# Performance work log

Hardware: AMD Instinct MI355X
Metric: run time of the kernel (lower is better)

Reference implementation:

```python
import math
import jax, jax.numpy as jnp
import numpy as np

V, D, H, L, F, T, B = 32000, 1024, 16, 4, 4096, 1024, 2
HD = D // H
EPS = 1e-5


def make_pe(max_len, d):
    pos = np.arange(max_len)[:, None].astype(np.float32)
    div = np.exp(np.arange(0, d, 2).astype(np.float32) * (-math.log(10000.0) / d))
    pe = np.zeros((max_len, d), dtype=np.float32)
    pe[:, 0::2] = np.sin(pos * div)
    pe[:, 1::2] = np.cos(pos * div)
    return jnp.asarray(pe)


def setup_inputs() -> dict:
    key = jax.random.key(0)
    ks = jax.random.split(key, 12)
    s = 0.02
    inp = {
        'tokens': jax.random.randint(ks[0], (B, T), 0, V, dtype=jnp.int32),
        'mask': jnp.tril(jnp.ones((T, T), dtype=jnp.int32)),
        'emb': jax.random.normal(ks[1], (V, D), jnp.float32) * s,
        'pe': make_pe(T, D),
        'ln1_g': jnp.ones((L, D)), 'ln1_b': jnp.zeros((L, D)),
        'Wqkv': jax.random.normal(ks[2], (L, D, 3 * D), jnp.float32) * s,
        'bqkv': jnp.zeros((L, 3 * D)),
        'Wproj': jax.random.normal(ks[3], (L, D, D), jnp.float32) * s,
        'bproj': jnp.zeros((L, D)),
        'ln2_g': jnp.ones((L, D)), 'ln2_b': jnp.zeros((L, D)),
        'W1': jax.random.normal(ks[4], (L, D, F), jnp.float32) * s,
        'b1': jnp.zeros((L, F)),
        'W2': jax.random.normal(ks[5], (L, F, D), jnp.float32) * s,
        'b2': jnp.zeros((L, D)),
        'lnf_g': jnp.ones((D,)), 'lnf_b': jnp.zeros((D,)),
        'out_b': jnp.zeros((V,)),
    }
    return inp


def layer_norm(x, g, b):
    m = jnp.mean(x, axis=-1, keepdims=True)
    v = jnp.mean((x - m) ** 2, axis=-1, keepdims=True)
    return (x - m) / jnp.sqrt(v + EPS) * g + b


def attention(x, mask, Wqkv, bqkv, Wproj, bproj):
    b, t, c = x.shape
    qkv = (x @ Wqkv + bqkv).reshape(b, t, 3, H, HD)
    q, k, v = jnp.moveaxis(qkv, 2, 0)  # each [B,T,H,HD]
    q = q.transpose(0, 2, 1, 3)  # [B,H,T,HD]
    k = k.transpose(0, 2, 1, 3)
    v = v.transpose(0, 2, 1, 3)
    scores = jnp.einsum('bhqd,bhkd->bhqk', q, k) / math.sqrt(HD)
    scores = jnp.where(mask[None, None] == 0, -1e9, scores)
    attn = jax.nn.softmax(scores, axis=-1)
    out = jnp.einsum('bhqk,bhkd->bhqd', attn, v)
    out = out.transpose(0, 2, 1, 3).reshape(b, t, c)
    return out @ Wproj + bproj, attn


def reference(tokens, mask, emb, pe, ln1_g, ln1_b, Wqkv, bqkv, Wproj, bproj,
              ln2_g, ln2_b, W1, b1, W2, b2, lnf_g, lnf_b, out_b):
    x = emb[tokens] + pe[:tokens.shape[1]]
    attn = None
    for i in range(L):
        a, attn = attention(layer_norm(x, ln1_g[i], ln1_b[i]), mask,
                            Wqkv[i], bqkv[i], Wproj[i], bproj[i])
        x = x + a
        h = layer_norm(x, ln2_g[i], ln2_b[i])
        h = jax.nn.gelu(h @ W1[i] + b1[i], approximate=False) @ W2[i] + b2[i]
        x = x + h
    x = layer_norm(x, lnf_g, lnf_b)
    logits = x @ emb.T + out_b  # weight tying
    return logits, attn
```

## Files before the change

### kernel.cpp

```cpp
#include <hip/hip_runtime.h>
#include <cstdint>

#define DEV static __device__ __forceinline__

typedef unsigned short u16;
typedef __bf16 bf16x8 __attribute__((ext_vector_type(8)));
typedef float f32x4 __attribute__((ext_vector_type(4)));
typedef unsigned short u16x4 __attribute__((ext_vector_type(4)));

constexpr int V = 32000, D = 1024, H = 16, L = 4, F = 4096, T = 1024, B = 2;
constexpr int HD = 64;

DEV u16 f2bf(float f) {
    union { float f; uint32_t i; } c; c.f = f;
    uint32_t x = c.i;
    return (u16)((x + 0x7fffu + ((x >> 16) & 1u)) >> 16);
}
DEV float bf2f(u16 u) {
    union { uint32_t i; float f; } c; c.i = ((uint32_t)u) << 16; return c.f;
}
DEV bf16x8 ld8(const u16* p) { return *reinterpret_cast<const bf16x8*>(p); }

DEV void gl16(const void* g, void* l) {
    __builtin_amdgcn_global_load_lds((const __attribute__((address_space(1))) void*)g,
                                     (__attribute__((address_space(3))) void*)l, 16, 0, 0);
}

DEV void castT4_dev(int t, int x, int y, u16 (*tl)[33],
        const float* __restrict__ Wqkv, const float* __restrict__ Wproj,
        const float* __restrict__ W1, const float* __restrict__ W2,
        u16* __restrict__ wt) {
    const float* src; u16* dst; int Rr, Cc;
    if (t < 768)       { src = Wqkv;  dst = wt;                       Rr = D; Cc = 3 * D; }
    else if (t < 1024) { src = Wproj; dst = wt + 3 * D * D;           Rr = D; Cc = D; t -= 768; }
    else if (t < 2048) { src = W1;    dst = wt + 4 * D * D;           Rr = D; Cc = F; t -= 1024; }
    else               { src = W2;    dst = wt + 4 * D * D + D * F;   Rr = F; Cc = D; t -= 2048; }
    int colStrips = Cc >> 7;
    int r0 = (t / colStrips) * 32;
    int c0 = (t % colStrips) * 128;
    for (int i = 0; i < 4; i++) {
        int cc = c0 + i * 32;
        __syncthreads();
#pragma unroll
        for (int j = 0; j < 4; j++)
            tl[y + j * 8][x] = f2bf(src[(size_t)(r0 + y + j * 8) * Cc + cc + x]);
        __syncthreads();
#pragma unroll
        for (int j = 0; j < 4; j++)
            dst[(size_t)(cc + y + j * 8) * Rr + r0 + x] = tl[x][y + j * 8];
    }
}

__global__ __launch_bounds__(256) void k_emblnT(const int* __restrict__ tok,
        const float* __restrict__ emb, const float* __restrict__ pe,
        const float* __restrict__ g, const float* __restrict__ b,
        float* __restrict__ x, u16* __restrict__ out,
        const float* __restrict__ Wqkv, const float* __restrict__ Wproj,
        const float* __restrict__ W1, const float* __restrict__ W2,
        u16* __restrict__ wt) {
    __shared__ u16 tl[32][33];
    __shared__ float ps[4], ps2[4];
    int row = blockIdx.x, tid = threadIdx.x;
    if (row >= B * T) {
        castT4_dev(row - B * T, tid & 31, tid >> 5, tl, Wqkv, Wproj, W1, W2, wt);
        return;
    }
    int t = row & (T - 1);
    int vv = tok[row];
    f32x4 v = ((const f32x4*)(emb + (size_t)vv * D))[tid] + ((const f32x4*)(pe + (size_t)t * D))[tid];
    ((f32x4*)(x + (size_t)row * D))[tid] = v;
    float s = v[0] + v[1] + v[2] + v[3];
    float s2 = v[0]*v[0] + v[1]*v[1] + v[2]*v[2] + v[3]*v[3];
#pragma unroll
    for (int m = 1; m < 64; m <<= 1) { s += __shfl_xor(s, m); s2 += __shfl_xor(s2, m); }
    int wave = tid >> 6;
    if ((tid & 63) == 0) { ps[wave] = s; ps2[wave] = s2; }
    __syncthreads();
    s = ps[0] + ps[1] + ps[2] + ps[3];
    s2 = ps2[0] + ps2[1] + ps2[2] + ps2[3];
    float mean = s * (1.f / D);
    float var = s2 * (1.f / D) - mean * mean;
    float r = rsqrtf(var + 1e-5f);
    f32x4 gg = ((const f32x4*)g)[tid];
    f32x4 bb = ((const f32x4*)b)[tid];
    u16x4 o;
#pragma unroll
    for (int j = 0; j < 4; j++) o[j] = f2bf((v[j] - mean) * r * gg[j] + bb[j]);
    ((u16x4*)(out + (size_t)row * D))[tid] = o;
}

template <int S, bool DOCAST>
__global__ __launch_bounds__(256) void k_redlnT(const u16* __restrict__ pp,
        const float* __restrict__ bias, float* __restrict__ x,
        const float* __restrict__ g, const float* __restrict__ b,
        u16* __restrict__ out,
        const float* __restrict__ Wqkv, const float* __restrict__ Wproj,
        const float* __restrict__ W1, const float* __restrict__ W2,
        u16* __restrict__ wt) {
    __shared__ u16 tl[32][33];
    __shared__ float ps[4], ps2[4];
    int row = blockIdx.x, tid = threadIdx.x;
    if (DOCAST && row >= B * T) {
        castT4_dev(row - B * T, tid & 31, tid >> 5, tl, Wqkv, Wproj, W1, W2, wt);
        return;
    }
    f32x4 v = ((const f32x4*)(x + (size_t)row * D))[tid];
#pragma unroll
    for (int s = 0; s < S; s++) {
        u16x4 pk = ((const u16x4*)(pp + ((size_t)s * (B * T) + row) * D))[tid];
#pragma unroll
        for (int j = 0; j < 4; j++) v[j] += bf2f(pk[j]);
    }
    v += ((const f32x4*)bias)[tid];
    ((f32x4*)(x + (size_t)row * D))[tid] = v;
    float s = v[0] + v[1] + v[2] + v[3];
    float s2 = v[0]*v[0] + v[1]*v[1] + v[2]*v[2] + v[3]*v[3];
#pragma unroll
    for (int m = 1; m < 64; m <<= 1) { s += __shfl_xor(s, m); s2 += __shfl_xor(s2, m); }
    int wave = tid >> 6;
    if ((tid & 63) == 0) { ps[wave] = s; ps2[wave] = s2; }
    __syncthreads();
    s = ps[0] + ps[1] + ps[2] + ps[3];
    s2 = ps2[0] + ps2[1] + ps2[2] + ps2[3];
    float mean = s * (1.f / D);
    float var = s2 * (1.f / D) - mean * mean;
    float r = rsqrtf(var + 1e-5f);
    f32x4 gg = ((const f32x4*)g)[tid];
    f32x4 bb = ((const f32x4*)b)[tid];
    u16x4 o;
#pragma unroll
    for (int j = 0; j < 4; j++) o[j] = f2bf((v[j] - mean) * r * gg[j] + bb[j]);
    ((u16x4*)(out + (size_t)row * D))[tid] = o;
}

DEV bf16x8 ldf(const u16* half, int row, int lhi) {
    int lb = row * 64 + lhi * 16;
    lb ^= ((lb >> 9) & 1) << 5;
    return *(const bf16x8*)((const char*)half + lb);
}
DEV void stg(const u16* gb, int ld, int kc, u16* dstBase, int wave, int lane) {
#pragma unroll
    for (int i = 0; i < 2; i++) {
        int p = (wave * 2 + i) * 64 + lane;
        int l = p ^ (((p >> 5) & 1) << 1);
        gl16(gb + (size_t)(l >> 2) * ld + kc + (l & 3) * 8, dstBase + (wave * 2 + i) * 512);
    }
}
#define SB_BAR() do { __builtin_amdgcn_sched_barrier(0); __builtin_amdgcn_s_barrier(); } while (0)

template <int EPI, bool VT>
__global__ __launch_bounds__(256, 2) void k_gemm4(
        const u16* __restrict__ A, int lda,
        const u16* __restrict__ Bt, int ldb,
        const float* __restrict__ bias,
        void* __restrict__ Cv, int ldc, int K, u16* __restrict__ vT) {
    __shared__ u16 lds[2][4][128 * 32];
    int gm = gridDim.x, nwg = gm * gridDim.y;
    int orig = blockIdx.y * gm + blockIdx.x;
    int xcd = orig & 7, idx = orig >> 3;
    int q = nwg >> 3, rr = nwg & 7;
    int wg = (xcd < rr ? xcd * (q + 1) : rr * (q + 1) + (xcd - rr) * q) + idx;
    int m0 = (wg % gm) * 128, n0 = (wg / gm) * 128;
    int koff = (EPI == 4) ? blockIdx.z * K : 0;
    int tid = threadIdx.x, wave = tid >> 6, lane = tid & 63;
    int llo = lane & 15, lhi = lane >> 4;
    int wm = wave >> 1, wn = wave & 1;
    const u16* Ab = A + (size_t)m0 * lda;
    const u16* Bb = Bt + (size_t)n0 * ldb;
    int nk = K >> 6;
    f32x4 acc[4][4] = {};
    stg(Ab, lda, koff + 0,   &lds[0][0][0], wave, lane);
    stg(Bb, ldb, koff + 0,   &lds[0][1][0], wave, lane);
    stg(Ab, lda, koff + 32,  &lds[0][2][0], wave, lane);
    stg(Bb, ldb, koff + 32,  &lds[0][3][0], wave, lane);
    stg(Ab, lda, koff + 64,  &lds[1][0][0], wave, lane);
    stg(Bb, ldb, koff + 64,  &lds[1][1][0], wave, lane);
    stg(Ab, lda, koff + 96,  &lds[1][2][0], wave, lane);
    asm volatile("s_waitcnt vmcnt(10)");
    SB_BAR();
    for (int t = 0; t < nk; ++t) {
        const int bf = t & 1;
        bf16x8 af[4], b0, b1;
#pragma unroll
        for (int mi = 0; mi < 4; mi++) af[mi] = ldf(&lds[bf][0][0], wm * 64 + mi * 16 + llo, lhi);
        b0 = ldf(&lds[bf][1][0], wn * 64 + llo, lhi);
        b1 = ldf(&lds[bf][1][0], wn * 64 + 16 + llo, lhi);
        if (t + 1 < nk) stg(Bb, ldb, koff + (t + 1) * 64 + 32, &lds[bf ^ 1][3][0], wave, lane);
        __builtin_amdgcn_s_setprio(1);
#pragma unroll
        for (int mi = 0; mi < 4; mi++) {
            acc[mi][0] = __builtin_amdgcn_mfma_f32_16x16x32_bf16(af[mi], b0, acc[mi][0], 0, 0, 0);
            acc[mi][1] = __builtin_amdgcn_mfma_f32_16x16x32_bf16(af[mi], b1, acc[mi][1], 0, 0, 0);
        }
        __builtin_amdgcn_s_setprio(0);
        SB_BAR();
        b0 = ldf(&lds[bf][1][0], wn * 64 + 32 + llo, lhi);
        b1 = ldf(&lds[bf][1][0], wn * 64 + 48 + llo, lhi);
        if (t + 2 < nk) stg(Ab, lda, koff + (t + 2) * 64, &lds[bf][0][0], wave, lane);
        __builtin_amdgcn_s_setprio(1);
#pragma unroll
        for (int mi = 0; mi < 4; mi++) {
            acc[mi][2] = __builtin_amdgcn_mfma_f32_16x16x32_bf16(af[mi], b0, acc[mi][2], 0, 0, 0);
            acc[mi][3] = __builtin_amdgcn_mfma_f32_16x16x32_bf16(af[mi], b1, acc[mi][3], 0, 0, 0);
        }
        __builtin_amdgcn_s_setprio(0);
        if (t + 2 < nk)      { asm volatile("s_waitcnt vmcnt(10)"); }
        else if (t + 1 < nk) { asm volatile("s_waitcnt vmcnt(8)"); }
        else                 { asm volatile("s_waitcnt vmcnt(0)"); }
        SB_BAR();
#pragma unroll
        for (int mi = 0; mi < 4; mi++) af[mi] = ldf(&lds[bf][2][0], wm * 64 + mi * 16 + llo, lhi);
        b0 = ldf(&lds[bf][3][0], wn * 64 + llo, lhi);
        b1 = ldf(&lds[bf][3][0], wn * 64 + 16 + llo, lhi);
        if (t + 2 < nk) stg(Bb, ldb, koff + (t + 2) * 64, &lds[bf][1][0], wave, lane);
        __builtin_amdgcn_s_setprio(1);
#pragma unroll
        for (int mi = 0; mi < 4; mi++) {
            acc[mi][0] = __builtin_amdgcn_mfma_f32_16x16x32_bf16(af[mi], b0, acc[mi][0], 0, 0, 0);
            acc[mi][1] = __builtin_amdgcn_mfma_f32_16x16x32_bf16(af[mi], b1, acc[mi][1], 0, 0, 0);
        }
        __builtin_amdgcn_s_setprio(0);
        SB_BAR();
        b0 = ldf(&lds[bf][3][0], wn * 64 + 32 + llo, lhi);
        b1 = ldf(&lds[bf][3][0], wn * 64 + 48 + llo, lhi);
        if (t + 2 < nk) stg(Ab, lda, koff + (t + 2) * 64 + 32, &lds[bf][2][0], wave, lane);
        __builtin_amdgcn_s_setprio(1);
#pragma unroll
        for (int mi = 0; mi < 4; mi++) {
            acc[mi][2] = __builtin_amdgcn_mfma_f32_16x16x32_bf16(af[mi], b0, acc[mi][2], 0, 0, 0);
            acc[mi][3] = __builtin_amdgcn_mfma_f32_16x16x32_bf16(af[mi], b1, acc[mi][3], 0, 0, 0);
        }
        __builtin_amdgcn_s_setprio(0);
        if (t + 1 < nk) {
            if (t + 2 < nk) { asm volatile("s_waitcnt vmcnt(10)"); }
            else            { asm volatile("s_waitcnt vmcnt(4)"); }
        }
        SB_BAR();
    }
#pragma unroll
    for (int ni = 0; ni < 4; ni++) {
        int col = n0 + wn * 64 + ni * 16 + llo;
        float bb = 0.f;
        if (EPI != 4) bb = bias[col];
#pragma unroll
        for (int mi = 0; mi < 4; mi++) {
            int row0 = m0 + wm * 64 + mi * 16 + lhi * 4;
            if (VT && col >= 2 * D) {
                int dv = col - 2 * D;
                int b_ = row0 >> 10, t_ = row0 & (T - 1);
                u16x4 pk;
#pragma unroll
                for (int r = 0; r < 4; r++) pk[r] = f2bf(acc[mi][ni][r] + bb);
                *(u16x4*)(vT + ((size_t)(b_ * 16 + (dv >> 6)) * HD + (dv & 63)) * T + t_) = pk;
            } else {
#pragma unroll
                for (int r = 0; r < 4; r++) {
                    int row = row0 + r;
                    float o = acc[mi][ni][r] + bb;
                    if (EPI == 1) o = 0.5f * o * (1.f + erff(o * 0.70710678118f));
                    if (EPI == 4) {
                        ((u16*)Cv)[((size_t)blockIdx.z * (B * T) + row) * ldc + col] = f2bf(o);
                    } else {
                        ((u16*)Cv)[(size_t)row * ldc + col] = f2bf(o);
                    }
                }
            }
        }
    }
}

__global__ __launch_bounds__(512, 2) void k_gemm8(
        const u16* __restrict__ A, int lda,
        const u16* __restrict__ Bt, int ldb,
        const float* __restrict__ bias,
        float* __restrict__ C, int ldc, int K) {
    __shared__ u16 lds[2][4][256 * 32];
    int gm = gridDim.x, nwg = gm * gridDim.y;
    int orig = blockIdx.y * gm + blockIdx.x;
    int xcd = orig & 7, idx = orig >> 3;
    int q = nwg >> 3, rr = nwg & 7;
    int wg = (xcd < rr ? xcd * (q + 1) : rr * (q + 1) + (xcd - rr) * q) + idx;
    int m0 = (wg % gm) * 256, n0 = (wg / gm) * 256;
    int tid = threadIdx.x, wave = tid >> 6, lane = tid & 63;
    int llo = lane & 15, lhi = lane >> 4;
    int wm = wave >> 2, wn = wave & 3;
    const u16* Ab = A + (size_t)m0 * lda;
    const u16* Bb = Bt + (size_t)n0 * ldb;
    int nk = K >> 6;
    f32x4 acc[8][4] = {};
    stg(Ab, lda, 0,   &lds[0][0][0], wave, lane);
    stg(Bb, ldb, 0,   &lds[0][1][0], wave, lane);
    stg(Ab, lda, 32,  &lds[0][2][0], wave, lane);
    stg(Bb, ldb, 32,  &lds[0][3][0], wave, lane);
    stg(Ab, lda, 64,  &lds[1][0][0], wave, lane);
    stg(Bb, ldb, 64,  &lds[1][1][0], wave, lane);
    stg(Ab, lda, 96,  &lds[1][2][0], wave, lane);
    asm volatile("s_waitcnt vmcnt(10)");
    SB_BAR();
    for (int t = 0; t < nk; ++t) {
        const int bf = t & 1;
        bf16x8 af[8], b0, b1;
#pragma unroll
        for (int mi = 0; mi < 8; mi++) af[mi] = ldf(&lds[bf][0][0], wm * 128 + mi * 16 + llo, lhi);
        b0 = ldf(&lds[bf][1][0], wn * 64 + llo, lhi);
        b1 = ldf(&lds[bf][1][0], wn * 64 + 16 + llo, lhi);
        if (t + 1 < nk) stg(Bb, ldb, (t + 1) * 64 + 32, &lds[bf ^ 1][3][0], wave, lane);
        __builtin_amdgcn_s_setprio(1);
#pragma unroll
        for (int mi = 0; mi < 8; mi++) {
            acc[mi][0] = __builtin_amdgcn_mfma_f32_16x16x32_bf16(af[mi], b0, acc[mi][0], 0, 0, 0);
            acc[mi][1] = __builtin_amdgcn_mfma_f32_16x16x32_bf16(af[mi], b1, acc[mi][1], 0, 0, 0);
        }
        __builtin_amdgcn_s_setprio(0);
        SB_BAR();
        b0 = ldf(&lds[bf][1][0], wn * 64 + 32 + llo, lhi);
        b1 = ldf(&lds[bf][1][0], wn * 64 + 48 + llo, lhi);
        if (t + 2 < nk) stg(Ab, lda, (t + 2) * 64, &lds[bf][0][0], wave, lane);
        __builtin_amdgcn_s_setprio(1);
#pragma unroll
        for (int mi = 0; mi < 8; mi++) {
            acc[mi][2] = __builtin_amdgcn_mfma_f32_16x16x32_bf16(af[mi], b0, acc[mi][2], 0, 0, 0);
            acc[mi][3] = __builtin_amdgcn_mfma_f32_16x16x32_bf16(af[mi], b1, acc[mi][3], 0, 0, 0);
        }
        __builtin_amdgcn_s_setprio(0);
        if (t + 2 < nk)      { asm volatile("s_waitcnt vmcnt(10)"); }
        else if (t + 1 < nk) { asm volatile("s_waitcnt vmcnt(8)"); }
        else                 { asm volatile("s_waitcnt vmcnt(0)"); }
        SB_BAR();
#pragma unroll
        for (int mi = 0; mi < 8; mi++) af[mi] = ldf(&lds[bf][2][0], wm * 128 + mi * 16 + llo, lhi);
        b0 = ldf(&lds[bf][3][0], wn * 64 + llo, lhi);
        b1 = ldf(&lds[bf][3][0], wn * 64 + 16 + llo, lhi);
        if (t + 2 < nk) stg(Bb, ldb, (t + 2) * 64, &lds[bf][1][0], wave, lane);
        __builtin_amdgcn_s_setprio(1);
#pragma unroll
        for (int mi = 0; mi < 8; mi++) {
            acc[mi][0] = __builtin_amdgcn_mfma_f32_16x16x32_bf16(af[mi], b0, acc[mi][0], 0, 0, 0);
            acc[mi][1] = __builtin_amdgcn_mfma_f32_16x16x32_bf16(af[mi], b1, acc[mi][1], 0, 0, 0);
        }
        __builtin_amdgcn_s_setprio(0);
        SB_BAR();
        b0 = ldf(&lds[bf][3][0], wn * 64 + 32 + llo, lhi);
        b1 = ldf(&lds[bf][3][0], wn * 64 + 48 + llo, lhi);
        if (t + 2 < nk) stg(Ab, lda, (t + 2) * 64 + 32, &lds[bf][2][0], wave, lane);
        __builtin_amdgcn_s_setprio(1);
#pragma unroll
        for (int mi = 0; mi < 8; mi++) {
            acc[mi][2] = __builtin_amdgcn_mfma_f32_16x16x32_bf16(af[mi], b0, acc[mi][2], 0, 0, 0);
            acc[mi][3] = __builtin_amdgcn_mfma_f32_16x16x32_bf16(af[mi], b1, acc[mi][3], 0, 0, 0);
        }
        __builtin_amdgcn_s_setprio(0);
        if (t + 1 < nk) {
            if (t + 2 < nk) { asm volatile("s_waitcnt vmcnt(10)"); }
            else            { asm volatile("s_waitcnt vmcnt(4)"); }
        }
        SB_BAR();
    }
#pragma unroll
    for (int ni = 0; ni < 4; ni++) {
        int col = n0 + wn * 64 + ni * 16 + llo;
        float bb = bias[col];
#pragma unroll
        for (int mi = 0; mi < 8; mi++) {
            int row0 = m0 + wm * 128 + mi * 16 + lhi * 4;
#pragma unroll
            for (int r = 0; r < 4; r++)
                C[(size_t)(row0 + r) * ldc + col] = acc[mi][ni][r] + bb;
        }
    }
}

template <int PW>
__global__ __launch_bounds__(256) void k_fattn(const u16* __restrict__ qkv,
        const u16* __restrict__ vT, u16* __restrict__ out, float* __restrict__ attnF,
        const float* __restrict__ embf, u16* __restrict__ embB, int castBase) {
    __shared__ u16 plds[4][16 * 40];
    int gid = blockIdx.x, tid = threadIdx.x;
    if (gid >= 512) {
        size_t base = ((size_t)castBase + (gid - 512)) * 16384;
        const f32x4* src = (const f32x4*)(embf + base);
        u16x4* dst = (u16x4*)(embB + base);
#pragma unroll 4
        for (int i = 0; i < 16; i++) {
            f32x4 v = src[i * 256 + tid];
            u16x4 o;
#pragma unroll
            for (int j = 0; j < 4; j++) o[j] = f2bf(v[j]);
            dst[i * 256 + tid] = o;
        }
        return;
    }
    int bh = gid >> 4; int b = bh >> 4, h = bh & 15;
    int wave = tid >> 6, lane = tid & 63;
    int llo = lane & 15, lhi = lane >> 4;
    int i0 = (gid & 15) * 64 + wave * 16;
    const u16* qb = qkv + (size_t)b * T * (3 * D) + h * HD;
    const u16* kb = qb + D;
    const u16* vt = vT + (size_t)bh * HD * T;
    bf16x8 q0 = ld8(qb + (size_t)(i0 + llo) * (3 * D) + lhi * 8);
    bf16x8 q1 = ld8(qb + (size_t)(i0 + llo) * (3 * D) + 32 + lhi * 8);
    int qrow = i0 + llo;
    float m = -3e38f, s = 0.f;
    f32x4 oacc[4] = {};
    u16* pw = &plds[wave][0];
    for (int k0 = 0; k0 < i0 + 16; k0 += 32) {
        f32x4 sc0 = {}, sc1 = {};
        {
            bf16x8 kf0 = ld8(kb + (size_t)(k0 + llo) * (3 * D) + lhi * 8);
            bf16x8 kf1 = ld8(kb + (size_t)(k0 + llo) * (3 * D) + 32 + lhi * 8);
            sc0 = __builtin_amdgcn_mfma_f32_16x16x32_bf16(kf0, q0, sc0, 0, 0, 0);
            sc0 = __builtin_amdgcn_mfma_f32_16x16x32_bf16(kf1, q1, sc0, 0, 0, 0);
        }
        if (k0 + 16 < i0 + 16) {
            bf16x8 kf0 = ld8(kb + (size_t)(k0 + 16 + llo) * (3 * D) + lhi * 8);
            bf16x8 kf1 = ld8(kb + (size_t)(k0 + 16 + llo) * (3 * D) + 32 + lhi * 8);
            sc1 = __builtin_amdgcn_mfma_f32_16x16x32_bf16(kf0, q0, sc1, 0, 0, 0);
            sc1 = __builtin_amdgcn_mfma_f32_16x16x32_bf16(kf1, q1, sc1, 0, 0, 0);
        }
        float vv[8]; float tmx = -3e38f;
#pragma unroll
        for (int hf = 0; hf < 2; hf++)
#pragma unroll
            for (int r = 0; r < 4; r++) {
                int k = k0 + hf * 16 + lhi * 4 + r;
                float x = (hf ? sc1[r] : sc0[r]) * 0.125f;
                float v = (k <= qrow) ? x : -3e38f;
                vv[hf * 4 + r] = v;
                tmx = fmaxf(tmx, v);
            }
        tmx = fmaxf(tmx, __shfl_xor(tmx, 16));
        tmx = fmaxf(tmx, __shfl_xor(tmx, 32));
        bool defer = __all(tmx <= m + 8.f);
        float nm = defer ? m : fmaxf(m, tmx);
        float p[8]; float ps = 0.f;
#pragma unroll
        for (int j = 0; j < 8; j++) { p[j] = __expf(vv[j] - nm); ps += p[j]; }
        ps += __shfl_xor(ps, 16);
        ps += __shfl_xor(ps, 32);
        if (!defer) {
            float scale = __expf(m - nm);
            s = s * scale + ps;
            m = nm;
            float sr[4];
#pragma unroll
            for (int r = 0; r < 4; r++) sr[r] = __shfl(scale, lhi * 4 + r);
#pragma unroll
            for (int n = 0; n < 4; n++)
#pragma unroll
                for (int r = 0; r < 4; r++) oacc[n][r] *= sr[r];
        } else {
            s += ps;
        }
#pragma unroll
        for (int hf = 0; hf < 2; hf++) {
            u16x4 pk;
#pragma unroll
            for (int r = 0; r < 4; r++) pk[r] = f2bf(p[hf * 4 + r]);
            *(u16x4*)(pw + llo * 40 + hf * 16 + lhi * 4) = pk;
        }
        bf16x8 pa = ld8(pw + llo * 40 + lhi * 8);
#pragma unroll
        for (int n = 0; n < 4; n++) {
            bf16x8 vb = ld8(vt + (size_t)(n * 16 + llo) * T + k0 + lhi * 8);
            oacc[n] = __builtin_amdgcn_mfma_f32_16x16x32_bf16(pa, vb, oacc[n], 0, 0, 0);
        }
    }
    float inv = 1.f / s;
    float ir[4];
#pragma unroll
    for (int r = 0; r < 4; r++) ir[r] = __shfl(inv, lhi * 4 + r);
#pragma unroll
    for (int n = 0; n < 4; n++)
#pragma unroll
        for (int r = 0; r < 4; r++) {
            int i = i0 + lhi * 4 + r, c = n * 16 + llo;
            out[(size_t)(b * T + i) * D + h * HD + c] = f2bf(oacc[n][r] * ir[r]);
        }
    if (PW) {
        float* ar = attnF + ((size_t)bh * T + qrow) * T;
        for (int j0 = 0; j0 < T; j0 += 16) {
            f32x4 pv = {};
            if (j0 <= qrow) {
                if (j0 < i0 + 16) {
                    bf16x8 kf0 = ld8(kb + (size_t)(j0 + llo) * (3 * D) + lhi * 8);
                    bf16x8 kf1 = ld8(kb + (size_t)(j0 + llo) * (3 * D) + 32 + lhi * 8);
                    f32x4 sc = {};
                    sc = __builtin_amdgcn_mfma_f32_16x16x32_bf16(kf0, q0, sc, 0, 0, 0);
                    sc = __builtin_amdgcn_mfma_f32_16x16x32_bf16(kf1, q1, sc, 0, 0, 0);
#pragma unroll
                    for (int r = 0; r < 4; r++) {
                        int j = j0 + lhi * 4 + r;
                        pv[r] = (j <= qrow) ? __expf(sc[r] * 0.125f - m) * inv : 0.f;
                    }
                }
            }
            *(f32x4*)(ar + j0 + lhi * 4) = pv;
        }
    }
}

extern "C" void kernel_launch(void* const* d_in, const int* in_sizes, int n_in,
                              void* d_out, int out_size, void* d_ws, size_t ws_size,
                              hipStream_t stream) {
    const int*   tok   = (const int*)d_in[0];
    const float* emb   = (const float*)d_in[2];
    const float* pe    = (const float*)d_in[3];
    const float* ln1g  = (const float*)d_in[4];
    const float* ln1b  = (const float*)d_in[5];
    const float* Wqkv  = (const float*)d_in[6];
    const float* bqkv  = (const float*)d_in[7];
    const float* Wproj = (const float*)d_in[8];
    const float* bproj = (const float*)d_in[9];
    const float* ln2g  = (const float*)d_in[10];
    const float* ln2b  = (const float*)d_in[11];
    const float* W1    = (const float*)d_in[12];
    const float* b1    = (const float*)d_in[13];
    const float* W2    = (const float*)d_in[14];
    const float* b2    = (const float*)d_in[15];
    const float* lnfg  = (const float*)d_in[16];
    const float* lnfb  = (const float*)d_in[17];
    const float* outb  = (const float*)d_in[18];

    float* logits  = (float*)d_out;
    float* attnF   = logits + (size_t)B * T * V;

    char* w = (char*)d_ws;
    float* x    = (float*)w;  w += (size_t)B * T * D * 4;
    u16* lnout  = (u16*)w;    w += (size_t)B * T * D * 2;
    u16* qkv    = (u16*)w;    w += (size_t)B * T * 3 * D * 2;
    u16* vT     = (u16*)w;    w += (size_t)B * H * HD * T * 2;
    u16* aout   = (u16*)w;    w += (size_t)B * T * D * 2;
    u16* hmid   = (u16*)w;    w += (size_t)B * T * F * 2;
    u16* WTL    = (u16*)w;    w += (size_t)(5 * D * D + 2 * D * F) * 2;
    u16* pp     = (u16*)w;    w += (size_t)4 * B * T * D * 2;
    u16* embB   = (u16*)w;    w += (size_t)V * D * 2;

    dim3 blk(256);
    const int CG = 3072;
    const int CC = 500;
    k_emblnT<<<dim3(B * T + CG), blk, 0, stream>>>(tok, emb, pe, ln1g, ln1b, x, lnout,
        Wqkv, Wproj, W1, W2, WTL);

    for (int l = 0; l < L; l++) {
        k_gemm4<0, true><<<dim3(B * T / 128, 3 * D / 128), blk, 0, stream>>>(
            lnout, D, WTL, D, bqkv + l * 3 * D, qkv, 3 * D, D, vT);
        if (l == L - 1)
            k_fattn<1><<<dim3(512 + CC), blk, 0, stream>>>(qkv, vT, aout, attnF,
                emb, embB, l * CC);
        else
            k_fattn<0><<<dim3(512 + CC), blk, 0, stream>>>(qkv, vT, aout, attnF,
                emb, embB, l * CC);
        k_gemm4<4, false><<<dim3(B * T / 128, D / 128, 4), blk, 0, stream>>>(
            aout, D, WTL + (size_t)3 * D * D, D, nullptr, pp, D, D / 4, nullptr);
        k_redlnT<4, false><<<dim3(B * T), blk, 0, stream>>>(pp, bproj + l * D, x,
            ln2g + l * D, ln2b + l * D, lnout, nullptr, nullptr, nullptr, nullptr, nullptr);
        k_gemm4<1, false><<<dim3(B * T / 128, F / 128), blk, 0, stream>>>(
            lnout, D, WTL + (size_t)4 * D * D, D, b1 + l * F, hmid, F, D, nullptr);
        k_gemm4<4, false><<<dim3(B * T / 128, D / 128, 4), blk, 0, stream>>>(
            hmid, F, WTL + (size_t)4 * D * D + D * F, F, nullptr, pp, D, F / 4, nullptr);
        if (l < L - 1) {
            k_redlnT<4, true><<<dim3(B * T + CG), blk, 0, stream>>>(pp, b2 + l * D, x,
                ln1g + (l + 1) * D, ln1b + (l + 1) * D, lnout,
                Wqkv + (size_t)(l + 1) * D * 3 * D, Wproj + (size_t)(l + 1) * D * D,
                W1 + (size_t)(l + 1) * D * F, W2 + (size_t)(l + 1) * F * D, WTL);
        } else {
            k_redlnT<4, false><<<dim3(B * T), blk, 0, stream>>>(pp, b2 + l * D, x,
                lnfg, lnfb, lnout, nullptr, nullptr, nullptr, nullptr, nullptr);
        }
    }
    k_gemm8<<<dim3(B * T / 256, V / 256), dim3(512), 0, stream>>>(
        lnout, D, embB, D, outb, logits, V, D);
}
```

Measured before the change: 959.0 us.

## Restructure GEMM K-loop into two phases with full-k fragment loads

The GEMM main loop goes from four barrier-separated sub-phases per 64-wide k step to two. In each phase both 32-wide k halves of A and B fragments are loaded at once and sixteen MFMAs are issued. B prefetch for the next step now happens entirely in the first phase and A prefetch for step t+2 in the second, with vmcnt waits adjusted to match. The aim is fewer workgroup barriers and longer MFMA runs. The cost is more live fragment registers and less staggering of the global loads.

```diff
diff --git a/kernel.cpp b/kernel.cpp
--- a/kernel.cpp
+++ b/kernel.cpp
@@ -174,66 +174,60 @@
     stg(Ab, lda, koff + 32,  &lds[0][2][0], wave, lane);
     stg(Bb, ldb, koff + 32,  &lds[0][3][0], wave, lane);
     stg(Ab, lda, koff + 64,  &lds[1][0][0], wave, lane);
-    stg(Bb, ldb, koff + 64,  &lds[1][1][0], wave, lane);
     stg(Ab, lda, koff + 96,  &lds[1][2][0], wave, lane);
-    asm volatile("s_waitcnt vmcnt(10)");
+    asm volatile("s_waitcnt vmcnt(4)");
     SB_BAR();
     for (int t = 0; t < nk; ++t) {
         const int bf = t & 1;
-        bf16x8 af[4], b0, b1;
-#pragma unroll
-        for (int mi = 0; mi < 4; mi++) af[mi] = ldf(&lds[bf][0][0], wm * 64 + mi * 16 + llo, lhi);
+        bf16x8 a0[4], a1[4], b0, b1, b2, b3;
+#pragma unroll
+        for (int mi = 0; mi < 4; mi++) a0[mi] = ldf(&lds[bf][0][0], wm * 64 + mi * 16 + llo, lhi);
+#pragma unroll
+        for (int mi = 0; mi < 4; mi++) a1[mi] = ldf(&lds[bf][2][0], wm * 64 + mi * 16 + llo, lhi);
         b0 = ldf(&lds[bf][1][0], wn * 64 + llo, lhi);
         b1 = ldf(&lds[bf][1][0], wn * 64 + 16 + llo, lhi);
-        if (t + 1 < nk) stg(Bb, ldb, koff + (t + 1) * 64 + 32, &lds[bf ^ 1][3][0], wave, lane);
+        b2 = ldf(&lds[bf][3][0], wn * 64 + llo, lhi);
+        b3 = ldf(&lds[bf][3][0], wn * 64 + 16 + llo, lhi);
+        if (t + 1 < nk) {
+            stg(Bb, ldb, koff + (t + 1) * 64,      &lds[bf ^ 1][1][0], wave, lane);
+            stg(Bb, ldb, koff + (t + 1) * 64 + 32, &lds[bf ^ 1][3][0], wave, lane);
+        }
         __builtin_amdgcn_s_setprio(1);
 #pragma unroll
         for (int mi = 0; mi < 4; mi++) {
-            acc[mi][0] = __builtin_amdgcn_mfma_f32_16x16x32_bf16(af[mi], b0, acc[mi][0], 0, 0, 0);
-            acc[mi][1] = __builtin_amdgcn_mfma_f32_16x16x32_bf16(af[mi], b1, acc[mi][1], 0, 0, 0);
+            acc[mi][0] = __builtin_amdgcn_mfma_f32_16x16x32_bf16(a0[mi], b0, acc[mi][0], 0, 0, 0);
+            acc[mi][1] = __builtin_amdgcn_mfma_f32_16x16x32_bf16(a0[mi], b1, acc[mi][1], 0, 0, 0);
+        }
+#pragma unroll
+        for (int mi = 0; mi < 4; mi++) {
+            acc[mi][0] = __builtin_amdgcn_mfma_f32_16x16x32_bf16(a1[mi], b2, acc[mi][0], 0, 0, 0);
+            acc[mi][1] = __builtin_amdgcn_mfma_f32_16x16x32_bf16(a1[mi], b3, acc[mi][1], 0, 0, 0);
         }
         __builtin_amdgcn_s_setprio(0);
         SB_BAR();
         b0 = ldf(&lds[bf][1][0], wn * 64 + 32 + llo, lhi);
         b1 = ldf(&lds[bf][1][0], wn * 64 + 48 + llo, lhi);
-        if (t + 2 < nk) stg(Ab, lda, koff + (t + 2) * 64, &lds[bf][0][0], wave, lane);
+        b2 = ldf(&lds[bf][3][0], wn * 64 + 32 + llo, lhi);
+        b3 = ldf(&lds[bf][3][0], wn * 64 + 48 + llo, lhi);
+        if (t + 2 < nk) {
+            stg(Ab, lda, koff + (t + 2) * 64,      &lds[bf][0][0], wave, lane);
+            stg(Ab, lda, koff + (t + 2) * 64 + 32, &lds[bf][2][0], wave, lane);
+        }
         __builtin_amdgcn_s_setprio(1);
 #pragma unroll
         for (int mi = 0; mi < 4; mi++) {
-            acc[mi][2] = __builtin_amdgcn_mfma_f32_16x16x32_bf16(af[mi], b0, acc[mi][2], 0, 0, 0);
-            acc[mi][3] = __builtin_amdgcn_mfma_f32_16x16x32_bf16(af[mi], b1, acc[mi][3], 0, 0, 0);
-        }
-        __builtin_amdgcn_s_setprio(0);
-        if (t + 2 < nk)      { asm volatile("s_waitcnt vmcnt(10)"); }
-        else if (t + 1 < nk) { asm volatile("s_waitcnt vmcnt(8)"); }
-        else                 { asm volatile("s_waitcnt vmcnt(0)"); }
-        SB_BAR();
-#pragma unroll
-        for (int mi = 0; mi < 4; mi++) af[mi] = ldf(&lds[bf][2][0], wm * 64 + mi * 16 + llo, lhi);
-        b0 = ldf(&lds[bf][3][0], wn * 64 + llo, lhi);
-        b1 = ldf(&lds[bf][3][0], wn * 64 + 16 + llo, lhi);
-        if (t + 2 < nk) stg(Bb, ldb, koff + (t + 2) * 64, &lds[bf][1][0], wave, lane);
-        __builtin_amdgcn_s_setprio(1);
+            acc[mi][2] = __builtin_amdgcn_mfma_f32_16x16x32_bf16(a0[mi], b0, acc[mi][2], 0, 0, 0);
+            acc[mi][3] = __builtin_amdgcn_mfma_f32_16x16x32_bf16(a0[mi], b1, acc[mi][3], 0, 0, 0);
+        }
 #pragma unroll
         for (int mi = 0; mi < 4; mi++) {
-            acc[mi][0] = __builtin_amdgcn_mfma_f32_16x16x32_bf16(af[mi], b0, acc[mi][0], 0, 0, 0);
-            acc[mi][1] = __builtin_amdgcn_mfma_f32_16x16x32_bf16(af[mi], b1, acc[mi][1], 0, 0, 0);
-        }
-        __builtin_amdgcn_s_setprio(0);
-        SB_BAR();
-        b0 = ldf(&lds[bf][3][0], wn * 64 + 32 + llo, lhi);
-        b1 = ldf(&lds[bf][3][0], wn * 64 + 48 + llo, lhi);
-        if (t + 2 < nk) stg(Ab, lda, koff + (t + 2) * 64 + 32, &lds[bf][2][0], wave, lane);
-        __builtin_amdgcn_s_setprio(1);
-#pragma unroll
-        for (int mi = 0; mi < 4; mi++) {
-            acc[mi][2] = __builtin_amdgcn_mfma_f32_16x16x32_bf16(af[mi], b0, acc[mi][2], 0, 0, 0);
-            acc[mi][3] = __builtin_amdgcn_mfma_f32_16x16x32_bf16(af[mi], b1, acc[mi][3], 0, 0, 0);
+            acc[mi][2] = __builtin_amdgcn_mfma_f32_16x16x32_bf16(a1[mi], b2, acc[mi][2], 0, 0, 0);
+            acc[mi][3] = __builtin_amdgcn_mfma_f32_16x16x32_bf16(a1[mi], b3, acc[mi][3], 0, 0, 0);
         }
         __builtin_amdgcn_s_setprio(0);
         if (t + 1 < nk) {
-            if (t + 2 < nk) { asm volatile("s_waitcnt vmcnt(10)"); }
-            else            { asm volatile("s_waitcnt vmcnt(4)"); }
+            if (t + 2 < nk) { asm volatile("s_waitcnt vmcnt(4)"); }
+            else            { asm volatile("s_waitcnt vmcnt(0)"); }
         }
         SB_BAR();
     }
```

After: 943.9 us. About the same (-1.6%).
